# Performance work log

Hardware: AMD Instinct MI355X
Metric: run time of the kernel (lower is better)

## Reference

```python
import jax, jax.numpy as jnp
import numpy as np


def setup_inputs() -> dict:
    key = jax.random.key(0)
    k1, k2 = jax.random.split(key)
    B, C, H, W, K = 8, 32, 224, 224, 5
    x = jax.random.normal(k1, (B, C, H, W), dtype=jnp.float32)
    kernel = jax.random.normal(k2, (C, 1, K, K), dtype=jnp.float32) * 0.1
    return {"x": x, "kernel": kernel, "stride": 1, "padding": 2, "dilation": 1}


def reference(x, kernel, stride, padding, dilation):
    # Tropical-max (morphological dilation) conv: out[p] = max_k (x[p+k] + w_flipped[k]).
    # is_max=True, softmax_temp=None -> hard max; kernel is flipped (true convolution).
    B, C, H, W = x.shape
    OC, _, K, _ = kernel.shape
    neutral = -jnp.inf
    x_pad = jnp.pad(x, ((0, 0), (0, 0), (padding, padding), (padding, padding)),
                    constant_values=neutral)
    Hp, Wp = H + 2 * padding, W + 2 * padding
    H_out = (Hp - dilation * (K - 1) - 1) // stride + 1
    W_out = (Wp - dilation * (K - 1) - 1) // stride + 1
    wflip = kernel[:, 0, ::-1, ::-1]  # (C, K, K) flipped, as in torch kernel.flip((2,3))
    # Start from neutral: matches the extra neutral row padded onto the unfold tensor.
    out = jnp.full((B, C, H_out, W_out), neutral, dtype=x.dtype)
    for i in range(K):  # small fixed K*K loop; avoids materializing the (B,C,K^2,HW) unfold
        for j in range(K):
            patch = x_pad[:, :,
                          i * dilation: i * dilation + (H_out - 1) * stride + 1: stride,
                          j * dilation: j * dilation + (W_out - 1) * stride + 1: stride]
            out = jnp.maximum(out, patch + wflip[:, i, j][None, :, None, None])
    return out
```

## Files before the change

### kernel.cpp

```cpp
#include <hip/hip_runtime.h>
#include <math.h>


#define TC_B 8
#define TC_C 32
#define TC_H 224
#define TC_W 224
#define TC_WQ 56
#define TC_HG 14

__global__ __launch_bounds__(256) void tropical_conv2d_kernel(
    const float* __restrict__ x, const float* __restrict__ kern,
    float* __restrict__ out) {
  const int tid = threadIdx.x;
  const int lane = tid & 63;
  const int yl = tid >> 6;
  const int blk = blockIdx.x;
  const int hg = blk % TC_HG;
  const int bc = blk / TC_HG;
  const int c = bc & (TC_C - 1);

  const float NEG = -INFINITY;

  float w[25];
  #pragma unroll
  for (int q = 0; q < 25; ++q) w[q] = kern[c * 25 + 24 - q];

  if (lane >= TC_WQ) return;

  const float* xp = x + (size_t)bc * (TC_H * TC_W);
  const int hbase = hg * 16 + yl * 4;

  float acc[4][4];
  #pragma unroll
  for (int o = 0; o < 4; ++o)
    #pragma unroll
    for (int k = 0; k < 4; ++k) acc[o][k] = NEG;

  const bool ledge = (lane == 0);
  const bool redge = (lane == TC_WQ - 1);
  const int col0 = lane * 4;

  #pragma unroll
  for (int ri = 0; ri < 8; ++ri) {
    const int g = hbase - 2 + ri;
    if (g < 0 || g >= TC_H) continue;
    const float* rowp = xp + (size_t)g * TC_W;

    const float4 Bv = *(const float4*)(rowp + col0);
    float2 A2, C2;
    if (ledge) { A2 = make_float2(NEG, NEG); }
    else       { A2 = *(const float2*)(rowp + col0 - 2); }
    if (redge) { C2 = make_float2(NEG, NEG); }
    else       { C2 = *(const float2*)(rowp + col0 + 4); }

    const float u[8] = {A2.x, A2.y, Bv.x, Bv.y, Bv.z, Bv.w, C2.x, C2.y};

    #pragma unroll
    for (int o = 0; o < 4; ++o) {
      const int i = ri - o;
      if (i < 0 || i > 4) continue;
      #pragma unroll
      for (int k = 0; k < 4; ++k) {
        const float m01 = fmaxf(u[k + 0] + w[i * 5 + 0],
                                u[k + 1] + w[i * 5 + 1]);
        const float m23 = fmaxf(u[k + 2] + w[i * 5 + 2],
                                u[k + 3] + w[i * 5 + 3]);
        const float m4  = u[k + 4] + w[i * 5 + 4];
        acc[o][k] = fmaxf(fmaxf(acc[o][k], m01), fmaxf(m23, m4));
      }
    }
  }

  float* op = out + (size_t)bc * (TC_H * TC_W) + (size_t)hbase * TC_W;
  #pragma unroll
  for (int o = 0; o < 4; ++o) {
    ((float4*)(op + (size_t)o * TC_W))[lane] =
        make_float4(acc[o][0], acc[o][1], acc[o][2], acc[o][3]);
  }
}

extern "C" void kernel_launch(void* const* d_in, const int* in_sizes, int n_in,
                              void* d_out, int out_size, void* d_ws, size_t ws_size,
                              hipStream_t stream) {
  const float* x = (const float*)d_in[0];
  const float* k = (const float*)d_in[1];
  float* out = (float*)d_out;

  dim3 block(256, 1, 1);
  dim3 grid(TC_B * TC_C * TC_HG, 1, 1);
  tropical_conv2d_kernel<<<grid, block, 0, stream>>>(x, k, out);
}
```

Measured before the change: 115.7 us.

## Stream rows through a rolling register window per 28-row strip

Each 64-thread wavefront now walks a 28-row strip and keeps a rolling 5-row register window, so every input row is loaded once instead of being reloaded for each 4-row output group (halo overhead drops from 8/4 to 32/28). Outputs are written with nontemporal stores, and block IDs are remapped so neighbouring strips of one image land on the same XCD. The trade-offs are fewer, longer-running workgroups with a serial dependency chain and more register pressure, which can cost latency hiding.

```diff
diff --git a/kernel.cpp b/kernel.cpp
--- a/kernel.cpp
+++ b/kernel.cpp
@@ -7,20 +7,58 @@
 #define TC_H 224
 #define TC_W 224
 #define TC_WQ 56
-#define TC_HG 14
+#define HS 28
+#define NSTRIP (TC_H / HS)
+#define NWG (TC_B * TC_C * NSTRIP)
+#define NXCD 8
+#define WPX (NWG / NXCD)
 
-__global__ __launch_bounds__(256) void tropical_conv2d_kernel(
+typedef float f4v __attribute__((ext_vector_type(4)));
+
+__device__ __forceinline__ void load_row(float* us, const float* __restrict__ xp,
+                                         int ga, int col0, bool ledge, bool redge) {
+  const float NEG = -INFINITY;
+  if (ga >= 0 && ga < TC_H) {
+    const float* rp = xp + (size_t)ga * TC_W + col0;
+    const float2 A2 = ledge ? make_float2(NEG, NEG) : *(const float2*)(rp - 2);
+    const float4 B4 = *(const float4*)(rp);
+    const float2 C2 = redge ? make_float2(NEG, NEG) : *(const float2*)(rp + 4);
+    us[0] = A2.x; us[1] = A2.y; us[2] = B4.x; us[3] = B4.y;
+    us[4] = B4.z; us[5] = B4.w; us[6] = C2.x; us[7] = C2.y;
+  } else {
+    #pragma unroll
+    for (int m = 0; m < 8; ++m) us[m] = NEG;
+  }
+}
+
+template <bool BIRTH>
+__device__ __forceinline__ void upd_row(float* a, const float* uu,
+                                        const float* w5) {
+  #pragma unroll
+  for (int k = 0; k < 4; ++k) {
+    const float t0 = uu[k + 0] + w5[0];
+    const float t1 = uu[k + 1] + w5[1];
+    const float t2 = uu[k + 2] + w5[2];
+    const float t3 = uu[k + 3] + w5[3];
+    const float t4 = uu[k + 4] + w5[4];
+    const float xm = fmaxf(fmaxf(t0, t1), t2);
+    const float ym = BIRTH ? fmaxf(t3, t4)
+                           : fmaxf(fmaxf(t3, t4), a[k]);
+    a[k] = fmaxf(xm, ym);
+  }
+}
+
+__global__ __launch_bounds__(64) void tropical_conv2d_kernel(
     const float* __restrict__ x, const float* __restrict__ kern,
     float* __restrict__ out) {
-  const int tid = threadIdx.x;
-  const int lane = tid & 63;
-  const int yl = tid >> 6;
-  const int blk = blockIdx.x;
-  const int hg = blk % TC_HG;
-  const int bc = blk / TC_HG;
+  const int lane = threadIdx.x;
+
+  const int orig = blockIdx.x;
+  const int blk = (orig & (NXCD - 1)) * WPX + (orig >> 3);
+
+  const int strip = blk & (NSTRIP - 1);
+  const int bc = blk >> 3;
   const int c = bc & (TC_C - 1);
-
-  const float NEG = -INFINITY;
 
   float w[25];
   #pragma unroll
@@ -28,55 +66,52 @@
 
   if (lane >= TC_WQ) return;
 
-  const float* xp = x + (size_t)bc * (TC_H * TC_W);
-  const int hbase = hg * 16 + yl * 4;
-
-  float acc[4][4];
-  #pragma unroll
-  for (int o = 0; o < 4; ++o)
-    #pragma unroll
-    for (int k = 0; k < 4; ++k) acc[o][k] = NEG;
-
   const bool ledge = (lane == 0);
   const bool redge = (lane == TC_WQ - 1);
   const int col0 = lane * 4;
+  const float* xp = x + (size_t)bc * (TC_H * TC_W);
+  const int r0 = strip * HS;
 
+  const float NEG = -INFINITY;
+  float u[5][8];
+  float acc[5][4];
   #pragma unroll
-  for (int ri = 0; ri < 8; ++ri) {
-    const int g = hbase - 2 + ri;
-    if (g < 0 || g >= TC_H) continue;
-    const float* rowp = xp + (size_t)g * TC_W;
+  for (int s = 0; s < 5; ++s)
+    #pragma unroll
+    for (int k = 0; k < 4; ++k) acc[s][k] = NEG;
 
-    const float4 Bv = *(const float4*)(rowp + col0);
-    float2 A2, C2;
-    if (ledge) { A2 = make_float2(NEG, NEG); }
-    else       { A2 = *(const float2*)(rowp + col0 - 2); }
-    if (redge) { C2 = make_float2(NEG, NEG); }
-    else       { C2 = *(const float2*)(rowp + col0 + 4); }
+  load_row(u[3], xp, r0 - 2, col0, ledge, redge);
+  load_row(u[4], xp, r0 - 1, col0, ledge, redge);
+  load_row(u[0], xp, r0 + 0, col0, ledge, redge);
+  load_row(u[1], xp, r0 + 1, col0, ledge, redge);
+  load_row(u[2], xp, r0 + 2, col0, ledge, redge);
 
-    const float u[8] = {A2.x, A2.y, Bv.x, Bv.y, Bv.z, Bv.w, C2.x, C2.y};
+  upd_row<true >(acc[0], u[3], &w[0]);
+  upd_row<false>(acc[0], u[4], &w[5]);
+  upd_row<true >(acc[1], u[4], &w[0]);
 
+  float* opb = out + (size_t)bc * (TC_H * TC_W) + (size_t)r0 * TC_W + col0;
+
+  #pragma unroll 1
+  for (int t = 0; t < 6; ++t) {
     #pragma unroll
-    for (int o = 0; o < 4; ++o) {
-      const int i = ri - o;
-      if (i < 0 || i > 4) continue;
-      #pragma unroll
-      for (int k = 0; k < 4; ++k) {
-        const float m01 = fmaxf(u[k + 0] + w[i * 5 + 0],
-                                u[k + 1] + w[i * 5 + 1]);
-        const float m23 = fmaxf(u[k + 2] + w[i * 5 + 2],
-                                u[k + 3] + w[i * 5 + 3]);
-        const float m4  = u[k + 4] + w[i * 5 + 4];
-        acc[o][k] = fmaxf(fmaxf(acc[o][k], m01), fmaxf(m23, m4));
+    for (int q = 0; q < 5; ++q) {
+      const int g = 5 * t + q;
+      if (g < 27) load_row(u[(q + 3) % 5], xp, r0 + g + 3, col0, ledge, redge);
+
+      upd_row<false>(acc[(q + 3) % 5], u[q], &w[20]);
+      upd_row<false>(acc[(q + 4) % 5], u[q], &w[15]);
+      upd_row<false>(acc[q],           u[q], &w[10]);
+      upd_row<false>(acc[(q + 1) % 5], u[q], &w[5]);
+
+      if (q >= 2 || t > 0) {
+        const float* a = acc[(q + 3) % 5];
+        f4v val = {a[0], a[1], a[2], a[3]};
+        __builtin_nontemporal_store(val, (f4v*)(opb + (size_t)(g - 2) * TC_W));
       }
+
+      upd_row<true>(acc[(q + 2) % 5], u[q], &w[0]);
     }
-  }
-
-  float* op = out + (size_t)bc * (TC_H * TC_W) + (size_t)hbase * TC_W;
-  #pragma unroll
-  for (int o = 0; o < 4; ++o) {
-    ((float4*)(op + (size_t)o * TC_W))[lane] =
-        make_float4(acc[o][0], acc[o][1], acc[o][2], acc[o][3]);
   }
 }
 
@@ -87,7 +122,7 @@
   const float* k = (const float*)d_in[1];
   float* out = (float*)d_out;
 
-  dim3 block(256, 1, 1);
-  dim3 grid(TC_B * TC_C * TC_HG, 1, 1);
+  dim3 block(64, 1, 1);
+  dim3 grid(NWG, 1, 1);
   tropical_conv2d_kernel<<<grid, block, 0, stream>>>(x, k, out);
 }
```

Measured after the change: 128.3 us. 1.11x slower.
